# Optimization experiments

Hardware: AMD Instinct MI355X
Metric: run time of the kernel (lower is better)

The kernel has to match this reference:

```python
import jax, jax.numpy as jnp
import numpy as np

E = 1024   # embedding_size
H = 16     # num_heads
DH = E // H


def setup_inputs() -> dict:
    key = jax.random.key(0)
    ks = jax.random.split(key, 11)
    B, S = 2, 2048
    std = 0.02
    return {
        "query": jax.random.normal(ks[0], (B, S, E), jnp.float32),
        "key": jax.random.normal(ks[1], (B, S, E), jnp.float32),
        "value": jax.random.normal(ks[2], (B, S, E), jnp.float32),
        "Wq": jax.random.normal(ks[3], (E, E), jnp.float32) * std,
        "bq": jnp.zeros((E,), jnp.float32),
        "Wk": jax.random.normal(ks[4], (E, E), jnp.float32) * std,
        "bk": jnp.zeros((E,), jnp.float32),
        "Wv": jax.random.normal(ks[5], (E, E), jnp.float32) * std,
        "bv": jnp.zeros((E,), jnp.float32),
        "Wo": jax.random.normal(ks[6], (E, E), jnp.float32) * std,
        "bo": jnp.zeros((E,), jnp.float32),
    }


def _split_heads(x, B, S):
    # [B,S,E] -> [B,H,S,DH]
    return x.reshape(B, S, H, DH).transpose(0, 2, 1, 3)


def reference(query, key, value, Wq, bq, Wk, bk, Wv, bv, Wo, bo):
    B, S, _ = query.shape
    # torch Linear: y = x @ W.T + b
    q = _split_heads(query @ Wq.T + bq, B, S)
    k = _split_heads(key @ Wk.T + bk, B, key.shape[1])
    v = _split_heads(value @ Wv.T + bv, B, value.shape[1])
    # naive unscaled attention (original has no 1/sqrt(d) factor)
    scores = jnp.einsum("bhsd,bhtd->bhst", q, k)  # [B,H,S,T]
    attn = jax.nn.softmax(scores, axis=-1)
    out = jnp.einsum("bhst,bhtd->bhsd", attn, v)  # [B,H,S,DH]
    out = out.transpose(0, 2, 1, 3).reshape(B, S, E)
    return out @ Wo.T + bo
```

## Files before the change

### kernel.cpp

```cpp
#include <hip/hip_runtime.h>
#include <hip/hip_bf16.h>

constexpr int kB   = 2;
constexpr int kS   = 2048;
constexpr int kE   = 1024;
constexpr int kH   = 16;
constexpr int kDH  = 64;
constexpr int kTok = kB * kS;

constexpr float kLog2e = 1.4426950408889634f;

typedef short bf16x8 __attribute__((ext_vector_type(8)));
typedef float f32x4  __attribute__((ext_vector_type(4)));
typedef unsigned int uint2v __attribute__((ext_vector_type(2)));

__device__ __forceinline__ float bf2f(unsigned short s) {
  union { unsigned int u; float f; } c; c.u = ((unsigned int)s) << 16; return c.f;
}
__device__ __forceinline__ unsigned short f2bf(float f) {
  union { float f; unsigned int u; } c; c.f = f;
  unsigned int u = c.u;
  u += 0x7fffu + ((u >> 16) & 1u);
  return (unsigned short)(u >> 16);
}

__device__ __forceinline__ unsigned cvtpk(float lo, float hi) {
  unsigned r;
  asm("v_cvt_pk_bf16_f32 %0, %1, %2" : "=v"(r) : "v"(lo), "v"(hi));
  return r;
}

__device__ __forceinline__ float fexp2(float x) {
  float r;
  asm("v_exp_f32 %0, %1" : "=v"(r) : "v"(x));
  return r;
}

__device__ __forceinline__ void gl_lds16(const unsigned short* g, unsigned short* l) {
  __builtin_amdgcn_global_load_lds(
      (const __attribute__((address_space(1))) unsigned int*)g,
      (__attribute__((address_space(3))) unsigned int*)l, 16, 0, 0);
}

__global__ void detect_dtype(const unsigned short* __restrict__ q, int* flag) {
  __shared__ int cnt;
  if (threadIdx.x == 0) cnt = 0;
  __syncthreads();
  int bad = 0;
  for (int i = threadIdx.x; i < 4096; i += 256) {
    unsigned int e = (q[i] >> 7) & 0xFF;
    if (e >= 0xC0) bad++;
  }
  atomicAdd(&cnt, bad);
  __syncthreads();
  if (threadIdx.x == 0) *flag = (cnt > 8) ? 1 : 0;
}

struct Seg { const void* src; unsigned short* dst; unsigned int n; unsigned int blk0; };
struct ConvArgs { Seg s[11]; float scale[11]; };

__global__ __launch_bounds__(256) void conv_all(ConvArgs a, const int* __restrict__ flag) {
  const unsigned int bid = blockIdx.x;
  int si = 0;
  #pragma unroll
  for (int i = 1; i < 11; ++i)
    if (bid >= a.s[i].blk0) si = i;
  const Seg sg = a.s[si];
  const float sc = a.scale[si];
  const int i0 = ((int)(bid - sg.blk0) * 256 + threadIdx.x) * 8;
  if (i0 >= (int)sg.n) return;
  if (*flag) {
    const float* s = (const float*)sg.src + i0;
    f32x4 f0 = *(const f32x4*)(s);
    f32x4 f1 = *(const f32x4*)(s + 4);
    bf16x8 v;
    #pragma unroll
    for (int j = 0; j < 4; ++j) v[j]     = (short)f2bf(f0[j] * sc);
    #pragma unroll
    for (int j = 0; j < 4; ++j) v[j + 4] = (short)f2bf(f1[j] * sc);
    *(bf16x8*)&sg.dst[i0] = v;
  } else {
    bf16x8 v = *(const bf16x8*)((const unsigned short*)sg.src + i0);
    if (sc != 1.0f) {
      #pragma unroll
      for (int j = 0; j < 8; ++j)
        v[j] = (short)f2bf(bf2f((unsigned short)v[j]) * sc);
    }
    *(bf16x8*)&sg.dst[i0] = v;
  }
}

__device__ __forceinline__ void gemm_core(
    const unsigned short* __restrict__ A,
    const unsigned short* __restrict__ W,
    int Kdim, int bM, int bN,
    unsigned short* As, unsigned short* Ws,
    f32x4 acc[4][4])
{
  const int tid  = threadIdx.x;
  const int lane = tid & 63;
  const int wv   = tid >> 6;
  const int wm   = (wv >> 1) * 64;
  const int wn   = (wv & 1) * 64;
  const int lr   = lane & 15;
  const int kq   = (lane >> 4) * 8;

  const int r0 = tid >> 2;
  const int c0 = (tid & 3) * 8;

  const unsigned short* Ag = A + (size_t)(bM + r0) * Kdim + c0;
  const unsigned short* Wg = W + (size_t)(bN + r0) * Kdim + c0;
  unsigned short* lA = &As[tid * 8];
  unsigned short* lW = &Ws[tid * 8];

  gl_lds16(Ag,                      lA);
  gl_lds16(Ag + (size_t)64 * Kdim,  lA + 2048);
  gl_lds16(Wg,                      lW);
  gl_lds16(Wg + (size_t)64 * Kdim,  lW + 2048);
  __syncthreads();

  for (int k0 = 0; k0 < Kdim; k0 += 32) {
    const int co = ((k0 >> 5) & 1) * 4096;
    if (k0 + 32 < Kdim) {
      const int no = co ^ 4096;
      gl_lds16(Ag + k0 + 32,                      lA + no);
      gl_lds16(Ag + (size_t)64 * Kdim + k0 + 32,  lA + no + 2048);
      gl_lds16(Wg + k0 + 32,                      lW + no);
      gl_lds16(Wg + (size_t)64 * Kdim + k0 + 32,  lW + no + 2048);
    }

    bf16x8 a[4], b[4];
    #pragma unroll
    for (int i = 0; i < 4; ++i)
      a[i] = *(const bf16x8*)&As[co + (wm + i * 16 + lr) * 32 + kq];
    #pragma unroll
    for (int i = 0; i < 4; ++i)
      b[i] = *(const bf16x8*)&Ws[co + (wn + i * 16 + lr) * 32 + kq];
    #pragma unroll
    for (int i = 0; i < 4; ++i)
      #pragma unroll
      for (int j = 0; j < 4; ++j)
        acc[i][j] = __builtin_amdgcn_mfma_f32_16x16x32_bf16(a[i], b[j], acc[i][j], 0, 0, 0);

    __syncthreads();
  }
}

__device__ __forceinline__ void gemm_core64(
    const unsigned short* __restrict__ A,
    const unsigned short* __restrict__ W,
    int Kdim, int bM, int bN,
    unsigned short* As, unsigned short* Ws,
    f32x4 acc[4][4])
{
  const int tid  = threadIdx.x;
  const int lane = tid & 63;
  const int wv   = tid >> 6;
  const int wm   = (wv >> 1) * 64;
  const int wn   = (wv & 1) * 64;
  const int lr   = lane & 15;
  const int kq   = (lane >> 4) * 8;

  const int r0 = tid >> 3;
  const int c0 = (tid & 7) * 8;

  const unsigned short* Ag = A + (size_t)(bM + r0) * Kdim + c0;
  const unsigned short* Wg = W + (size_t)(bN + r0) * Kdim + c0;
  unsigned short* lA = &As[tid * 8];
  unsigned short* lW = &Ws[tid * 8];

  #pragma unroll
  for (int j = 0; j < 4; ++j) {
    gl_lds16(Ag + (size_t)(32 * j) * Kdim, lA + j * 2048);
    gl_lds16(Wg + (size_t)(32 * j) * Kdim, lW + j * 2048);
  }
  __syncthreads();

  for (int k0 = 0; k0 < Kdim; k0 += 64) {
    const int co = ((k0 >> 6) & 1) * 8192;
    if (k0 + 64 < Kdim) {
      const int no = co ^ 8192;
      #pragma unroll
      for (int j = 0; j < 4; ++j) {
        gl_lds16(Ag + (size_t)(32 * j) * Kdim + k0 + 64, lA + no + j * 2048);
        gl_lds16(Wg + (size_t)(32 * j) * Kdim + k0 + 64, lW + no + j * 2048);
      }
    }
    #pragma unroll
    for (int kk2 = 0; kk2 < 2; ++kk2) {
      bf16x8 a[4], b[4];
      #pragma unroll
      for (int i = 0; i < 4; ++i)
        a[i] = *(const bf16x8*)&As[co + (wm + i * 16 + lr) * 64 + kk2 * 32 + kq];
      #pragma unroll
      for (int i = 0; i < 4; ++i)
        b[i] = *(const bf16x8*)&Ws[co + (wn + i * 16 + lr) * 64 + kk2 * 32 + kq];
      #pragma unroll
      for (int i = 0; i < 4; ++i)
        #pragma unroll
        for (int j = 0; j < 4; ++j)
          acc[i][j] = __builtin_amdgcn_mfma_f32_16x16x32_bf16(a[i], b[j], acc[i][j], 0, 0, 0);
    }
    __syncthreads();
  }
}

__global__ __launch_bounds__(256) void gemm_qkv(
    const unsigned short* __restrict__ Abase,
    const unsigned short* __restrict__ Wbase,
    const unsigned short* __restrict__ biasbase,
    unsigned short* __restrict__ Cbase)
{
  __shared__ unsigned short As[2 * 128 * 32];
  __shared__ unsigned short Ws[2 * 128 * 32];

  const int bid = blockIdx.x + (blockIdx.y << 3) + (blockIdx.z << 8);
  const int swz = (bid & 7) * 96 + (bid >> 3);
  const int z   = swz >> 8;
  const int rem = swz & 255;
  const int bM  = (rem >> 3) * 128;
  const int bN  = (rem & 7) * 128;

  const unsigned short* A    = Abase    + (size_t)z * (kTok * kE);
  const unsigned short* W    = Wbase    + (size_t)z * (kE * kE);
  const unsigned short* bias = biasbase + (size_t)z * kE;
  unsigned short* C          = Cbase    + (size_t)z * (kTok * kE);

  f32x4 acc[4][4] = {};
  gemm_core(A, W, kE, bM, bN, As, Ws, acc);

  const int lane = threadIdx.x & 63;
  const int wv   = threadIdx.x >> 6;
  const int wm   = (wv >> 1) * 64;
  const int wn   = (wv & 1) * 64;
  const int lr   = lane & 15;
  const int qd   = lane >> 4;
  #pragma unroll
  for (int j = 0; j < 4; ++j) {
    const int col = bN + wn + j * 16 + lr;
    const float bb = bf2f(bias[col]);
    #pragma unroll
    for (int i = 0; i < 4; ++i)
      #pragma unroll
      for (int r = 0; r < 4; ++r) {
        const int row = bM + wm + i * 16 + qd * 4 + r;
        C[(size_t)row * kE + col] = f2bf(acc[i][j][r] + bb);
      }
  }
}

__global__ __launch_bounds__(256) void vtrans(
    const unsigned short* __restrict__ Vb,
    unsigned short* __restrict__ Vt)
{
  __shared__ unsigned short Lt[64 * 72];
  const int tid = threadIdx.x;
  const int bh  = blockIdx.y;
  const int b   = bh >> 4;
  const int h   = bh & 15;
  const int hcol = h * kDH;
  const int s0  = blockIdx.x * 64;

  #pragma unroll
  for (int issue = 0; issue < 2; ++issue) {
    int g = issue * 256 + tid;
    int r = g >> 3, c = (g & 7) * 8;
    bf16x8 vv = *(const bf16x8*)&Vb[(size_t)(b * kS + s0 + r) * kE + hcol + c];
    const int swz = ((((r >> 3) ^ (c >> 3)) & 7) << 3) + (r & 7);
    #pragma unroll
    for (int i = 0; i < 8; ++i)
      Lt[(c + i) * 72 + swz] = (unsigned short)vv[i];
  }
  __syncthreads();
  #pragma unroll
  for (int issue = 0; issue < 2; ++issue) {
    int g = issue * 256 + tid;
    int f = g >> 3, tc = (g & 7) * 8;
    const int blk = ((tc >> 3) ^ (f >> 3)) & 7;
    bf16x8 vv = *(const bf16x8*)&Lt[f * 72 + (blk << 3)];
    *(bf16x8*)&Vt[(size_t)b * (kE * kS) + (size_t)(hcol + f) * kS + s0 + tc] = vv;
  }
}

__global__ __launch_bounds__(256) void gemm_out(
    const unsigned short* __restrict__ A,
    const unsigned short* __restrict__ W,
    const unsigned short* __restrict__ bias,
    void* __restrict__ C,
    const int* __restrict__ flag)
{
  __shared__ unsigned short As[2 * 128 * 64];
  __shared__ unsigned short Ws[2 * 128 * 64];

  const int bid = blockIdx.x + (blockIdx.y << 3);
  const int swz = (bid & 7) * 32 + (bid >> 3);
  const int bM  = (swz >> 3) * 128;
  const int bN  = (swz & 7) * 128;

  f32x4 acc[4][4] = {};
  gemm_core64(A, W, kE, bM, bN, As, Ws, acc);

  const int lane = threadIdx.x & 63;
  const int wv   = threadIdx.x >> 6;
  const int wm   = (wv >> 1) * 64;
  const int wn   = (wv & 1) * 64;
  const int lr   = lane & 15;
  const int qd   = lane >> 4;
  if (*flag) {
    float* Cf = (float*)C;
    #pragma unroll
    for (int j = 0; j < 4; ++j) {
      const int col = bN + wn + j * 16 + lr;
      const float bb = bf2f(bias[col]);
      #pragma unroll
      for (int i = 0; i < 4; ++i)
        #pragma unroll
        for (int r = 0; r < 4; ++r) {
          const int row = bM + wm + i * 16 + qd * 4 + r;
          Cf[(size_t)row * kE + col] = acc[i][j][r] + bb;
        }
    }
  } else {
    unsigned short* Cb = (unsigned short*)C;
    #pragma unroll
    for (int j = 0; j < 4; ++j) {
      const int col = bN + wn + j * 16 + lr;
      const float bb = bf2f(bias[col]);
      #pragma unroll
      for (int i = 0; i < 4; ++i)
        #pragma unroll
        for (int r = 0; r < 4; ++r) {
          const int row = bM + wm + i * 16 + qd * 4 + r;
          Cb[(size_t)row * kE + col] = f2bf(acc[i][j][r] + bb);
        }
    }
  }
}

__global__ __launch_bounds__(256) void attn(
    const unsigned short* __restrict__ Qb,
    const unsigned short* __restrict__ Kb,
    const unsigned short* __restrict__ Vt,
    unsigned short* __restrict__ Ob)
{
  __shared__ unsigned short Ks[2][128 * 72];
  __shared__ unsigned short Vs[2][64 * 136];

  const int tid  = threadIdx.x;
  const int lane = tid & 63;
  const int w    = tid >> 6;
  const int lr   = lane & 15;
  const int quad = lane >> 4;
  const int kq   = quad * 8;

  const int bid = blockIdx.x + (blockIdx.y << 4);
  const int swz = (bid & 7) * 64 + (bid >> 3);
  const int bh  = swz >> 4;
  const int b   = bh >> 4;
  const int h   = bh & 15;
  const int q0  = (swz & 15) * 128;

  const size_t rowbase = (size_t)b * kS * kE;
  const int hcol = h * kDH;
  const unsigned short* Vbase = Vt + (size_t)b * (kE * kS) + (size_t)hcol * kS;

  const int kr = tid >> 3;
  const int kc = (tid & 7) * 8;
  const int vr = tid >> 2;
  const int vc = (tid & 3) * 8;

  bf16x8 aq[2][2];
  #pragma unroll
  for (int rg = 0; rg < 2; ++rg)
    #pragma unroll
    for (int hh = 0; hh < 2; ++hh)
      aq[rg][hh] = *(const bf16x8*)
          &Qb[rowbase + (size_t)(q0 + w * 32 + rg * 16 + lr) * kE + hcol + hh * 32 + kq];

  f32x4 o[2][4] = {};
  float l4[2][4] = {};

  bf16x8 rk[4], rv[4];
  #pragma unroll
  for (int j = 0; j < 4; ++j) {
    rk[j] = *(const bf16x8*)&Kb[rowbase + (size_t)(kr + 32 * j) * kE + hcol + kc];
    rv[j] = *(const bf16x8*)&Vbase[(size_t)vr * kS + vc + 32 * j];
  }
  #pragma unroll
  for (int j = 0; j < 4; ++j) {
    *(bf16x8*)&Ks[0][(kr + 32 * j) * 72 + kc] = rk[j];
    *(bf16x8*)&Vs[0][vr * 136 + vc + 32 * j]  = rv[j];
  }
  #pragma unroll
  for (int j = 0; j < 4; ++j) {
    rk[j] = *(const bf16x8*)&Kb[rowbase + (size_t)(128 + kr + 32 * j) * kE + hcol + kc];
    rv[j] = *(const bf16x8*)&Vbase[(size_t)vr * kS + 128 + vc + 32 * j];
  }
  __syncthreads();

  for (int t0 = 0; t0 < kS; t0 += 128) {
    const int cur = (t0 >> 7) & 1;
    const int nxt = cur ^ 1;

    if (t0 + 128 < kS) {
      #pragma unroll
      for (int j = 0; j < 4; ++j) {
        *(bf16x8*)&Ks[nxt][(kr + 32 * j) * 72 + kc] = rk[j];
        *(bf16x8*)&Vs[nxt][vr * 136 + vc + 32 * j]  = rv[j];
      }
    }
    if (t0 + 256 < kS) {
      const int t2 = t0 + 256;
      #pragma unroll
      for (int j = 0; j < 4; ++j) {
        rk[j] = *(const bf16x8*)&Kb[rowbase + (size_t)(t2 + kr + 32 * j) * kE + hcol + kc];
        rv[j] = *(const bf16x8*)&Vbase[(size_t)vr * kS + t2 + vc + 32 * j];
      }
    }

    f32x4 s[2][8];
    #pragma unroll
    for (int rg = 0; rg < 2; ++rg)
      #pragma unroll
      for (int tn = 0; tn < 8; ++tn)
        s[rg][tn] = f32x4{0.f, 0.f, 0.f, 0.f};
    __builtin_amdgcn_s_setprio(1);
    #pragma unroll
    for (int tn = 0; tn < 8; ++tn) {
      const bf16x8 bk0 = *(const bf16x8*)&Ks[cur][(tn * 16 + lr) * 72 + 0 + kq];
      const bf16x8 bk1 = *(const bf16x8*)&Ks[cur][(tn * 16 + lr) * 72 + 32 + kq];
      #pragma unroll
      for (int rg = 0; rg < 2; ++rg) {
        s[rg][tn] = __builtin_amdgcn_mfma_f32_16x16x32_bf16(bk0, aq[rg][0], s[rg][tn], 0, 0, 0);
        s[rg][tn] = __builtin_amdgcn_mfma_f32_16x16x32_bf16(bk1, aq[rg][1], s[rg][tn], 0, 0, 0);
      }
    }
    __builtin_amdgcn_s_setprio(0);

    #pragma unroll
    for (int rg = 0; rg < 2; ++rg)
      #pragma unroll
      for (int tn = 0; tn < 8; ++tn)
        #pragma unroll
        for (int r = 0; r < 4; ++r) {
          const float e = fexp2(s[rg][tn][r]);
          s[rg][tn][r] = e;
          l4[rg][r] += e;
        }

    bf16x8 ap[2][4];
    #pragma unroll
    for (int rg = 0; rg < 2; ++rg)
      #pragma unroll
      for (int kk = 0; kk < 4; ++kk) {
        const unsigned A0 = cvtpk(s[rg][2 * kk][0],     s[rg][2 * kk][1]);
        const unsigned A1 = cvtpk(s[rg][2 * kk + 1][0], s[rg][2 * kk + 1][1]);
        const uint2v u   = __builtin_amdgcn_permlane32_swap(A0, A1, false, false);
        const uint2v z02 = __builtin_amdgcn_permlane16_swap(u[0], u[1], false, false);
        const unsigned B0 = cvtpk(s[rg][2 * kk][2],     s[rg][2 * kk][3]);
        const unsigned B1 = cvtpk(s[rg][2 * kk + 1][2], s[rg][2 * kk + 1][3]);
        const uint2v v2  = __builtin_amdgcn_permlane32_swap(B0, B1, false, false);
        const uint2v z13 = __builtin_amdgcn_permlane16_swap(v2[0], v2[1], false, false);
        union { unsigned ud[4]; bf16x8 v; } pk;
        pk.ud[0] = z02[0];
        pk.ud[1] = z13[0];
        pk.ud[2] = z02[1];
        pk.ud[3] = z13[1];
        ap[rg][kk] = pk.v;
      }

    __builtin_amdgcn_s_setprio(1);
    #pragma unroll
    for (int kk = 0; kk < 4; ++kk)
      #pragma unroll
      for (int dt = 0; dt < 4; ++dt) {
        const bf16x8 bv = *(const bf16x8*)&Vs[cur][(dt * 16 + lr) * 136 + kk * 32 + kq];
        #pragma unroll
        for (int rg = 0; rg < 2; ++rg)
          o[rg][dt] = __builtin_amdgcn_mfma_f32_16x16x32_bf16(ap[rg][kk], bv, o[rg][dt], 0, 0, 0);
      }
    __builtin_amdgcn_s_setprio(0);

    __syncthreads();
  }

  #pragma unroll
  for (int rg = 0; rg < 2; ++rg) {
    float l = (l4[rg][0] + l4[rg][1]) + (l4[rg][2] + l4[rg][3]);
    l += __shfl_xor(l, 16, 64);
    l += __shfl_xor(l, 32, 64);
    float inv[4];
    #pragma unroll
    for (int r = 0; r < 4; ++r)
      inv[r] = 1.0f / __shfl(l, quad * 4 + r, 64);

    #pragma unroll
    for (int dt = 0; dt < 4; ++dt) {
      #pragma unroll
      for (int r = 0; r < 4; ++r) {
        const int row = q0 + w * 32 + rg * 16 + quad * 4 + r;
        const int col = hcol + dt * 16 + lr;
        Ob[rowbase + (size_t)row * kE + col] = f2bf(o[rg][dt][r] * inv[r]);
      }
    }
  }
}

extern "C" void kernel_launch(void* const* d_in, const int* in_sizes, int n_in,
                              void* d_out, int out_size, void* d_ws, size_t ws_size,
                              hipStream_t stream) {
  const int nQKV = kTok * kE;
  const int nW   = kE * kE;
  const int nB   = kE;

  char* wsb = (char*)d_ws;
  int* flag = (int*)wsb;
  unsigned short* qc  = (unsigned short*)(wsb + 16);
  unsigned short* kc  = qc  + (size_t)nQKV;
  unsigned short* vc  = kc  + (size_t)nQKV;
  unsigned short* Wqc = vc  + (size_t)nQKV;
  unsigned short* Wkc = Wqc + (size_t)nW;
  unsigned short* Wvc = Wkc + (size_t)nW;
  unsigned short* Woc = Wvc + (size_t)nW;
  unsigned short* bqc = Woc + (size_t)nW;
  unsigned short* bkc = bqc + nB;
  unsigned short* bvc = bkc + nB;
  unsigned short* boc = bvc + nB;
  unsigned short* Qb  = boc + nB;
  unsigned short* Kb  = Qb  + (size_t)nQKV;
  unsigned short* Vb  = Kb  + (size_t)nQKV;
  unsigned short* Vtb = kc;
  unsigned short* Ob  = qc;

  detect_dtype<<<1, 256, 0, stream>>>((const unsigned short*)d_in[0], flag);

  ConvArgs ca;
  const void* srcs[11] = { d_in[0], d_in[1], d_in[2], d_in[3], d_in[4], d_in[5],
                           d_in[6], d_in[7], d_in[8], d_in[9], d_in[10] };
  unsigned short* dsts[11] = { qc, kc, vc, Wqc, bqc, Wkc, bkc, Wvc, bvc, Woc, boc };
  const unsigned int ns[11] = { (unsigned)nQKV, (unsigned)nQKV, (unsigned)nQKV,
                                (unsigned)nW, (unsigned)nB, (unsigned)nW, (unsigned)nB,
                                (unsigned)nW, (unsigned)nB, (unsigned)nW, (unsigned)nB };
  unsigned int blk = 0;
  for (int i = 0; i < 11; ++i) {
    ca.s[i].src = srcs[i]; ca.s[i].dst = dsts[i]; ca.s[i].n = ns[i]; ca.s[i].blk0 = blk;
    ca.scale[i] = 1.0f;
    blk += (ns[i] + 2047) / 2048;
  }
  ca.scale[3] = kLog2e;
  ca.scale[4] = kLog2e;
  conv_all<<<blk, 256, 0, stream>>>(ca, flag);

  dim3 blk256(256);
  dim3 gqkv(kE / 128, kTok / 128, 3);
  gemm_qkv<<<gqkv, blk256, 0, stream>>>(qc, Wqc, bqc, Qb);

  dim3 gvt(kS / 64, kB * kH);
  vtrans<<<gvt, blk256, 0, stream>>>(Vb, Vtb);

  dim3 gattn(kS / 128, kB * kH);
  attn<<<gattn, blk256, 0, stream>>>(Qb, Kb, Vtb, Ob);

  dim3 gout(kE / 128, kTok / 128);
  gemm_out<<<gout, blk256, 0, stream>>>(Ob, Woc, boc, d_out, flag);
}
```

Measured before the change: 244.7 us.

## Triple-buffer GEMM LDS tiles with two-stage-ahead async prefetch

Converts the double-buffered global-to-LDS pipeline in both GEMM cores (QKV and output projection) into a three-stage ring. Loads are issued two k-steps ahead, and partial vmcnt waits replace the full __syncthreads, so one load batch stays in flight across each barrier. This is meant to hide global memory latency behind MFMA work. In exchange it uses 1.5x the LDS, which can lower occupancy (the out GEMM rises to 96KB), and it depends on correct manual waitcnt accounting.

```diff
diff --git a/kernel.cpp b/kernel.cpp
--- a/kernel.cpp
+++ b/kernel.cpp
@@ -113,20 +113,27 @@
   unsigned short* lA = &As[tid * 8];
   unsigned short* lW = &Ws[tid * 8];
 
-  gl_lds16(Ag,                      lA);
-  gl_lds16(Ag + (size_t)64 * Kdim,  lA + 2048);
-  gl_lds16(Wg,                      lW);
-  gl_lds16(Wg + (size_t)64 * Kdim,  lW + 2048);
-  __syncthreads();
-
+  gl_lds16(Ag,                           lA);
+  gl_lds16(Ag + (size_t)64 * Kdim,       lA + 2048);
+  gl_lds16(Wg,                           lW);
+  gl_lds16(Wg + (size_t)64 * Kdim,       lW + 2048);
+  gl_lds16(Ag + 32,                      lA + 4096);
+  gl_lds16(Ag + (size_t)64 * Kdim + 32,  lA + 4096 + 2048);
+  gl_lds16(Wg + 32,                      lW + 4096);
+  gl_lds16(Wg + (size_t)64 * Kdim + 32,  lW + 4096 + 2048);
+  asm volatile("s_waitcnt vmcnt(4)" ::: "memory");
+  __builtin_amdgcn_s_barrier();
+
+  int cur = 0;
   for (int k0 = 0; k0 < Kdim; k0 += 32) {
-    const int co = ((k0 >> 5) & 1) * 4096;
-    if (k0 + 32 < Kdim) {
-      const int no = co ^ 4096;
-      gl_lds16(Ag + k0 + 32,                      lA + no);
-      gl_lds16(Ag + (size_t)64 * Kdim + k0 + 32,  lA + no + 2048);
-      gl_lds16(Wg + k0 + 32,                      lW + no);
-      gl_lds16(Wg + (size_t)64 * Kdim + k0 + 32,  lW + no + 2048);
+    const int co = cur * 4096;
+    const bool issue = (k0 + 64 < Kdim);
+    if (issue) {
+      const int no = (cur == 0 ? 2 : cur - 1) * 4096;
+      gl_lds16(Ag + k0 + 64,                      lA + no);
+      gl_lds16(Ag + (size_t)64 * Kdim + k0 + 64,  lA + no + 2048);
+      gl_lds16(Wg + k0 + 64,                      lW + no);
+      gl_lds16(Wg + (size_t)64 * Kdim + k0 + 64,  lW + no + 2048);
     }
 
     bf16x8 a[4], b[4];
@@ -142,7 +149,12 @@
       for (int j = 0; j < 4; ++j)
         acc[i][j] = __builtin_amdgcn_mfma_f32_16x16x32_bf16(a[i], b[j], acc[i][j], 0, 0, 0);
 
-    __syncthreads();
+    if (issue)
+      asm volatile("s_waitcnt vmcnt(4)" ::: "memory");
+    else
+      asm volatile("s_waitcnt vmcnt(0)" ::: "memory");
+    __builtin_amdgcn_s_barrier();
+    cur = (cur == 2) ? 0 : cur + 1;
   }
 }
 
@@ -174,16 +186,24 @@
     gl_lds16(Ag + (size_t)(32 * j) * Kdim, lA + j * 2048);
     gl_lds16(Wg + (size_t)(32 * j) * Kdim, lW + j * 2048);
   }
-  __syncthreads();
-
+  #pragma unroll
+  for (int j = 0; j < 4; ++j) {
+    gl_lds16(Ag + (size_t)(32 * j) * Kdim + 64, lA + 8192 + j * 2048);
+    gl_lds16(Wg + (size_t)(32 * j) * Kdim + 64, lW + 8192 + j * 2048);
+  }
+  asm volatile("s_waitcnt vmcnt(8)" ::: "memory");
+  __builtin_amdgcn_s_barrier();
+
+  int cur = 0;
   for (int k0 = 0; k0 < Kdim; k0 += 64) {
-    const int co = ((k0 >> 6) & 1) * 8192;
-    if (k0 + 64 < Kdim) {
-      const int no = co ^ 8192;
+    const int co = cur * 8192;
+    const bool issue = (k0 + 128 < Kdim);
+    if (issue) {
+      const int no = (cur == 0 ? 2 : cur - 1) * 8192;
       #pragma unroll
       for (int j = 0; j < 4; ++j) {
-        gl_lds16(Ag + (size_t)(32 * j) * Kdim + k0 + 64, lA + no + j * 2048);
-        gl_lds16(Wg + (size_t)(32 * j) * Kdim + k0 + 64, lW + no + j * 2048);
+        gl_lds16(Ag + (size_t)(32 * j) * Kdim + k0 + 128, lA + no + j * 2048);
+        gl_lds16(Wg + (size_t)(32 * j) * Kdim + k0 + 128, lW + no + j * 2048);
       }
     }
     #pragma unroll
@@ -201,7 +221,12 @@
         for (int j = 0; j < 4; ++j)
           acc[i][j] = __builtin_amdgcn_mfma_f32_16x16x32_bf16(a[i], b[j], acc[i][j], 0, 0, 0);
     }
-    __syncthreads();
+    if (issue)
+      asm volatile("s_waitcnt vmcnt(8)" ::: "memory");
+    else
+      asm volatile("s_waitcnt vmcnt(0)" ::: "memory");
+    __builtin_amdgcn_s_barrier();
+    cur = (cur == 2) ? 0 : cur + 1;
   }
 }
 
@@ -211,8 +236,8 @@
     const unsigned short* __restrict__ biasbase,
     unsigned short* __restrict__ Cbase)
 {
-  __shared__ unsigned short As[2 * 128 * 32];
-  __shared__ unsigned short Ws[2 * 128 * 32];
+  __shared__ unsigned short As[3 * 128 * 32];
+  __shared__ unsigned short Ws[3 * 128 * 32];
 
   const int bid = blockIdx.x + (blockIdx.y << 3) + (blockIdx.z << 8);
   const int swz = (bid & 7) * 96 + (bid >> 3);
@@ -289,8 +314,8 @@
     void* __restrict__ C,
     const int* __restrict__ flag)
 {
-  __shared__ unsigned short As[2 * 128 * 64];
-  __shared__ unsigned short Ws[2 * 128 * 64];
+  __shared__ unsigned short As[3 * 128 * 64];
+  __shared__ unsigned short Ws[3 * 128 * 64];
 
   const int bid = blockIdx.x + (blockIdx.y << 3);
   const int swz = (bid & 7) * 32 + (bid >> 3);
```

New measurement: 246.8 us. No clear change (+0.9%).

## Fuse fp32-to-bf16 activation conversion into QKV projection GEMM loads

Applied to the files above, without the earlier changes.

The QKV GEMM now reads the raw query/key/value inputs and converts them to bf16 in registers while loading A tiles, so conv_all only converts the weights and biases. This removes a full pass that wrote and re-read three 4096x1024 activation tensors. In exchange, the A operand goes through register prefetch and explicit LDS stores instead of direct global-to-LDS loads, which adds register pressure and VALU conversion work inside the GEMM loop. Each activation tile is also re-converted by every N-block (8 times).

```diff
diff --git a/kernel.cpp b/kernel.cpp
--- a/kernel.cpp
+++ b/kernel.cpp
@@ -57,13 +57,13 @@
 }
 
 struct Seg { const void* src; unsigned short* dst; unsigned int n; unsigned int blk0; };
-struct ConvArgs { Seg s[11]; float scale[11]; };
+struct ConvArgs { Seg s[8]; float scale[8]; };
 
 __global__ __launch_bounds__(256) void conv_all(ConvArgs a, const int* __restrict__ flag) {
   const unsigned int bid = blockIdx.x;
   int si = 0;
   #pragma unroll
-  for (int i = 1; i < 11; ++i)
+  for (int i = 1; i < 8; ++i)
     if (bid >= a.s[i].blk0) si = i;
   const Seg sg = a.s[si];
   const float sc = a.scale[si];
@@ -90,13 +90,31 @@
   }
 }
 
-__device__ __forceinline__ void gemm_core(
-    const unsigned short* __restrict__ A,
-    const unsigned short* __restrict__ W,
-    int Kdim, int bM, int bN,
-    unsigned short* As, unsigned short* Ws,
-    f32x4 acc[4][4])
+__global__ __launch_bounds__(256) void gemm_qkv(
+    const void* __restrict__ Qraw, const void* __restrict__ Kraw,
+    const void* __restrict__ Vraw,
+    const unsigned short* __restrict__ Wbase,
+    const unsigned short* __restrict__ biasbase,
+    unsigned short* __restrict__ Cbase,
+    const int* __restrict__ flag)
 {
+  __shared__ unsigned short As[2 * 128 * 32];
+  __shared__ unsigned short Ws[2 * 128 * 32];
+
+  const int bid = blockIdx.x + (blockIdx.y << 3) + (blockIdx.z << 8);
+  const int swz = (bid & 7) * 96 + (bid >> 3);
+  const int z   = swz >> 8;
+  const int rem = swz & 255;
+  const int bM  = (rem >> 3) * 128;
+  const int bN  = (rem & 7) * 128;
+
+  const void* Ar = (z == 0) ? Qraw : (z == 1) ? Kraw : Vraw;
+  const unsigned short* W    = Wbase    + (size_t)z * (kE * kE);
+  const unsigned short* bias = biasbase + (size_t)z * kE;
+  unsigned short* C          = Cbase    + (size_t)z * (kTok * kE);
+
+  const bool isf32 = (*flag != 0);
+
   const int tid  = threadIdx.x;
   const int lane = tid & 63;
   const int wv   = tid >> 6;
@@ -104,30 +122,56 @@
   const int wn   = (wv & 1) * 64;
   const int lr   = lane & 15;
   const int kq   = (lane >> 4) * 8;
-
-  const int r0 = tid >> 2;
-  const int c0 = (tid & 3) * 8;
-
-  const unsigned short* Ag = A + (size_t)(bM + r0) * Kdim + c0;
-  const unsigned short* Wg = W + (size_t)(bN + r0) * Kdim + c0;
+  const int r0   = tid >> 2;
+  const int c0   = (tid & 3) * 8;
+
+  const unsigned short* Wg = W + (size_t)(bN + r0) * kE + c0;
+  unsigned short* lW = &Ws[tid * 8];
   unsigned short* lA = &As[tid * 8];
-  unsigned short* lW = &Ws[tid * 8];
-
-  gl_lds16(Ag,                      lA);
-  gl_lds16(Ag + (size_t)64 * Kdim,  lA + 2048);
-  gl_lds16(Wg,                      lW);
-  gl_lds16(Wg + (size_t)64 * Kdim,  lW + 2048);
+
+  const float*          Af = (const float*)Ar          + (size_t)(bM + r0) * kE + c0;
+  const unsigned short* Ab = (const unsigned short*)Ar + (size_t)(bM + r0) * kE + c0;
+
+  auto loadA = [&](int kk, bf16x8& lo, bf16x8& hi) {
+    if (isf32) {
+      f32x4 a0 = *(const f32x4*)(Af + kk);
+      f32x4 a1 = *(const f32x4*)(Af + kk + 4);
+      f32x4 b0 = *(const f32x4*)(Af + (size_t)64 * kE + kk);
+      f32x4 b1 = *(const f32x4*)(Af + (size_t)64 * kE + kk + 4);
+      #pragma unroll
+      for (int j = 0; j < 4; ++j) {
+        lo[j]     = (short)f2bf(a0[j]);
+        lo[j + 4] = (short)f2bf(a1[j]);
+        hi[j]     = (short)f2bf(b0[j]);
+        hi[j + 4] = (short)f2bf(b1[j]);
+      }
+    } else {
+      lo = *(const bf16x8*)(Ab + kk);
+      hi = *(const bf16x8*)(Ab + (size_t)64 * kE + kk);
+    }
+  };
+
+  bf16x8 rlo, rhi;
+  loadA(0, rlo, rhi);
+  *(bf16x8*)lA          = rlo;
+  *(bf16x8*)(lA + 2048) = rhi;
+  gl_lds16(Wg,                    lW);
+  gl_lds16(Wg + (size_t)64 * kE,  lW + 2048);
+  loadA(32, rlo, rhi);
   __syncthreads();
 
-  for (int k0 = 0; k0 < Kdim; k0 += 32) {
+  f32x4 acc[4][4] = {};
+  for (int k0 = 0; k0 < kE; k0 += 32) {
     const int co = ((k0 >> 5) & 1) * 4096;
-    if (k0 + 32 < Kdim) {
-      const int no = co ^ 4096;
-      gl_lds16(Ag + k0 + 32,                      lA + no);
-      gl_lds16(Ag + (size_t)64 * Kdim + k0 + 32,  lA + no + 2048);
-      gl_lds16(Wg + k0 + 32,                      lW + no);
-      gl_lds16(Wg + (size_t)64 * Kdim + k0 + 32,  lW + no + 2048);
-    }
+    const int no = co ^ 4096;
+    if (k0 + 32 < kE) {
+      *(bf16x8*)(lA + no)        = rlo;
+      *(bf16x8*)(lA + no + 2048) = rhi;
+      gl_lds16(Wg + k0 + 32,                    lW + no);
+      gl_lds16(Wg + (size_t)64 * kE + k0 + 32,  lW + no + 2048);
+    }
+    if (k0 + 64 < kE)
+      loadA(k0 + 64, rlo, rhi);
 
     bf16x8 a[4], b[4];
     #pragma unroll
@@ -143,6 +187,20 @@
         acc[i][j] = __builtin_amdgcn_mfma_f32_16x16x32_bf16(a[i], b[j], acc[i][j], 0, 0, 0);
 
     __syncthreads();
+  }
+
+  const int qd = lane >> 4;
+  #pragma unroll
+  for (int j = 0; j < 4; ++j) {
+    const int col = bN + wn + j * 16 + lr;
+    const float bb = bf2f(bias[col]);
+    #pragma unroll
+    for (int i = 0; i < 4; ++i)
+      #pragma unroll
+      for (int r = 0; r < 4; ++r) {
+        const int row = bM + wm + i * 16 + qd * 4 + r;
+        C[(size_t)row * kE + col] = f2bf(acc[i][j][r] + bb);
+      }
   }
 }
 
@@ -202,50 +260,6 @@
           acc[i][j] = __builtin_amdgcn_mfma_f32_16x16x32_bf16(a[i], b[j], acc[i][j], 0, 0, 0);
     }
     __syncthreads();
-  }
-}
-
-__global__ __launch_bounds__(256) void gemm_qkv(
-    const unsigned short* __restrict__ Abase,
-    const unsigned short* __restrict__ Wbase,
-    const unsigned short* __restrict__ biasbase,
-    unsigned short* __restrict__ Cbase)
-{
-  __shared__ unsigned short As[2 * 128 * 32];
-  __shared__ unsigned short Ws[2 * 128 * 32];
-
-  const int bid = blockIdx.x + (blockIdx.y << 3) + (blockIdx.z << 8);
-  const int swz = (bid & 7) * 96 + (bid >> 3);
-  const int z   = swz >> 8;
-  const int rem = swz & 255;
-  const int bM  = (rem >> 3) * 128;
-  const int bN  = (rem & 7) * 128;
-
-  const unsigned short* A    = Abase    + (size_t)z * (kTok * kE);
-  const unsigned short* W    = Wbase    + (size_t)z * (kE * kE);
-  const unsigned short* bias = biasbase + (size_t)z * kE;
-  unsigned short* C          = Cbase    + (size_t)z * (kTok * kE);
-
-  f32x4 acc[4][4] = {};
-  gemm_core(A, W, kE, bM, bN, As, Ws, acc);
-
-  const int lane = threadIdx.x & 63;
-  const int wv   = threadIdx.x >> 6;
-  const int wm   = (wv >> 1) * 64;
-  const int wn   = (wv & 1) * 64;
-  const int lr   = lane & 15;
-  const int qd   = lane >> 4;
-  #pragma unroll
-  for (int j = 0; j < 4; ++j) {
-    const int col = bN + wn + j * 16 + lr;
-    const float bb = bf2f(bias[col]);
-    #pragma unroll
-    for (int i = 0; i < 4; ++i)
-      #pragma unroll
-      for (int r = 0; r < 4; ++r) {
-        const int row = bM + wm + i * 16 + qd * 4 + r;
-        C[(size_t)row * kE + col] = f2bf(acc[i][j][r] + bb);
-      }
   }
 }
 
@@ -535,25 +549,25 @@
   detect_dtype<<<1, 256, 0, stream>>>((const unsigned short*)d_in[0], flag);
 
   ConvArgs ca;
-  const void* srcs[11] = { d_in[0], d_in[1], d_in[2], d_in[3], d_in[4], d_in[5],
-                           d_in[6], d_in[7], d_in[8], d_in[9], d_in[10] };
-  unsigned short* dsts[11] = { qc, kc, vc, Wqc, bqc, Wkc, bkc, Wvc, bvc, Woc, boc };
-  const unsigned int ns[11] = { (unsigned)nQKV, (unsigned)nQKV, (unsigned)nQKV,
-                                (unsigned)nW, (unsigned)nB, (unsigned)nW, (unsigned)nB,
-                                (unsigned)nW, (unsigned)nB, (unsigned)nW, (unsigned)nB };
+  const void* srcs[8] = { d_in[3], d_in[4], d_in[5], d_in[6],
+                          d_in[7], d_in[8], d_in[9], d_in[10] };
+  unsigned short* dsts[8] = { Wqc, bqc, Wkc, bkc, Wvc, bvc, Woc, boc };
+  const unsigned int ns[8] = { (unsigned)nW, (unsigned)nB, (unsigned)nW, (unsigned)nB,
+                               (unsigned)nW, (unsigned)nB, (unsigned)nW, (unsigned)nB };
   unsigned int blk = 0;
-  for (int i = 0; i < 11; ++i) {
+  for (int i = 0; i < 8; ++i) {
     ca.s[i].src = srcs[i]; ca.s[i].dst = dsts[i]; ca.s[i].n = ns[i]; ca.s[i].blk0 = blk;
     ca.scale[i] = 1.0f;
     blk += (ns[i] + 2047) / 2048;
   }
-  ca.scale[3] = kLog2e;
-  ca.scale[4] = kLog2e;
+  ca.scale[0] = kLog2e;
+  ca.scale[1] = kLog2e;
   conv_all<<<blk, 256, 0, stream>>>(ca, flag);
 
   dim3 blk256(256);
   dim3 gqkv(kE / 128, kTok / 128, 3);
-  gemm_qkv<<<gqkv, blk256, 0, stream>>>(qc, Wqc, bqc, Qb);
+  gemm_qkv<<<gqkv, blk256, 0, stream>>>(d_in[0], d_in[1], d_in[2],
+                                        Wqc, bqc, Qb, flag);
 
   dim3 gvt(kS / 64, kB * kH);
   vtrans<<<gvt, blk256, 0, stream>>>(Vb, Vtb);
```

Result: slower. 265.8 us (+8.6%).
